# Kernel optimization log

Measured on AMD Instinct MI355X. Metric: run time of the kernel, lower is better.

The kernel has to match this reference:

```python
import jax, jax.numpy as jnp
import numpy as np

NEG_SLOPE = 0.2  # PyG GATv2Conv default
TOPK = 10        # hard-coded in original forward


def setup_inputs() -> dict:
    key = jax.random.key(0)
    N, E, D, L = 50000, 640000, 128, 3
    ks = jax.random.split(key, 12)
    s = 1.0 / np.sqrt(D)
    x = jax.random.normal(ks[0], (N, D), jnp.float32)
    edge_index = jax.random.randint(ks[1], (2, E), 0, N, dtype=jnp.int64)
    edge_attributes = jax.random.normal(ks[2], (E, D), jnp.float32)
    # GATv2 per-layer params (heads=1): lin_l (src), lin_r (dst), lin_edge, att, out bias
    Wl = jax.random.normal(ks[3], (L, D, D), jnp.float32) * s
    bl = jnp.zeros((L, D), jnp.float32)
    Wr = jax.random.normal(ks[4], (L, D, D), jnp.float32) * s
    br = jnp.zeros((L, D), jnp.float32)
    We = jax.random.normal(ks[5], (L, D, D), jnp.float32) * s
    att = jax.random.normal(ks[6], (L, D), jnp.float32) * s
    bias = jnp.zeros((L, D), jnp.float32)
    # final Conv1d(D, 1, 1) == linear projection D -> 1 per node
    Wf = jax.random.normal(ks[7], (D, 1), jnp.float32) * s
    bf = jnp.zeros((1,), jnp.float32)
    return {"x": x, "edge_index": edge_index, "edge_attributes": edge_attributes,
            "Wl": Wl, "bl": bl, "Wr": Wr, "br": br, "We": We, "att": att,
            "bias": bias, "Wf": Wf, "bf": bf}


def _gatv2_layer(x, src, dst, ea, N, Wl, bl, Wr, br, We, att, bias):
    xl = x @ Wl + bl            # [N, D] source transform
    xr = x @ Wr + br            # [N, D] target transform
    ee = ea @ We                # [E', D] edge transform (no bias in PyG lin_edge)
    m = jax.nn.leaky_relu(xl[src] + xr[dst] + ee, NEG_SLOPE)  # [E', D]
    logits = m @ att            # [E']
    # per-destination softmax (every node has a self-loop -> no empty segments)
    mx = jax.ops.segment_max(logits, dst, num_segments=N)
    w = jnp.exp(logits - mx[dst])
    den = jax.ops.segment_sum(w, dst, num_segments=N)
    alpha = w / den[dst]
    out = jax.ops.segment_sum(xl[src] * alpha[:, None], dst, num_segments=N)
    return out + bias


def reference(x, edge_index, edge_attributes, Wl, bl, Wr, br, We, att, bias, Wf, bf):
    N, D = x.shape
    src, dst = edge_index[0], edge_index[1]
    loop = jnp.arange(N, dtype=src.dtype)
    # add_self_loops with fill_value='mean': loop attr = mean of incoming edge attrs
    cnt = jax.ops.segment_sum(jnp.ones_like(dst, dtype=x.dtype), dst, num_segments=N)
    loop_attr = jax.ops.segment_sum(edge_attributes, dst, num_segments=N) / jnp.maximum(cnt, 1.0)[:, None]
    src_f = jnp.concatenate([src, loop])
    dst_f = jnp.concatenate([dst, loop])
    ea = jnp.concatenate([edge_attributes, loop_attr], axis=0)
    L = Wl.shape[0]
    for i in range(L):
        x = _gatv2_layer(x, src_f, dst_f, ea, N, Wl[i], bl[i], Wr[i], br[i], We[i], att[i], bias[i])
    scores = (x @ Wf)[:, 0] + bf[0]   # Conv1d(D,1,1): per-node scalar score [N]
    vals, idx = jax.lax.top_k(scores, TOPK)
    return vals, idx
```

## Files before the change

kernel.cpp:

```cpp
#include <hip/hip_runtime.h>
#include <hip/hip_bf16.h>
#include <float.h>

#define DD 128
#define NEG_SLOPE 0.2f
#define TKB 128

typedef __attribute__((ext_vector_type(8))) short bf16x8;
typedef __attribute__((ext_vector_type(4))) float f32x4;

__device__ __forceinline__ float lrelu(float v) {
    return fmaxf(v, 0.0f) + NEG_SLOPE * fminf(v, 0.0f);
}

__device__ __forceinline__ unsigned short f2bf(float f) {
    unsigned u = __float_as_uint(f);
    u += 0x7fff + ((u >> 16) & 1);
    return (unsigned short)(u >> 16);
}
__device__ __forceinline__ float bf2f(unsigned short h) {
    return __uint_as_float(((unsigned)h) << 16);
}


__global__ void k_hist(const int* __restrict__ dst, int E, int* __restrict__ cnt) {
    int i = blockIdx.x * blockDim.x + threadIdx.x;
    if (i < E) atomicAdd(&cnt[dst[i]], 1);
}

__global__ __launch_bounds__(1024) void k_scan(const int* __restrict__ cnt,
                                               int* __restrict__ row_ptr, int N) {
    __shared__ int sums[1024];
    int tid = threadIdx.x;
    int total = N + 1;
    int chunk = (total + 1023) / 1024;
    int lo = tid * chunk;
    int hi = min(lo + chunk, total);
    int s = 0;
    for (int i = lo; i < hi; ++i) s += (i < N) ? (cnt[i] + 1) : 0;
    sums[tid] = s;
    __syncthreads();
    for (int off = 1; off < 1024; off <<= 1) {
        int t = (tid >= off) ? sums[tid - off] : 0;
        __syncthreads();
        sums[tid] += t;
        __syncthreads();
    }
    int run = sums[tid] - s;
    for (int i = lo; i < hi; ++i) {
        row_ptr[i] = run;
        run += (i < N) ? (cnt[i] + 1) : 0;
    }
}

__global__ void k_scatter(const int* __restrict__ dst, int E, int N,
                          const int* __restrict__ row_ptr, int* __restrict__ fill,
                          const int* __restrict__ cnt, int* __restrict__ eids) {
    int i = blockIdx.x * blockDim.x + threadIdx.x;
    int tot = E + N;
    if (i >= tot) return;
    if (i < E) {
        int d = dst[i];
        int p = atomicAdd(&fill[d], 1);
        eids[row_ptr[d] + p] = i;
    } else {
        int n = i - E;
        eids[row_ptr[n] + cnt[n]] = E + n;
    }
}

__global__ void k_sort_rows(const int* __restrict__ row_ptr, int* __restrict__ eids, int N) {
    int n = blockIdx.x * blockDim.x + threadIdx.x;
    if (n >= N) return;
    int s = row_ptr[n], e = row_ptr[n + 1];
    for (int i = s + 1; i < e; ++i) {
        int v = eids[i];
        int j = i - 1;
        while (j >= s && eids[j] > v) { eids[j + 1] = eids[j]; --j; }
        eids[j + 1] = v;
    }
}

__global__ void k_invert(const int* __restrict__ eids, const int* __restrict__ srcArr,
                         int* __restrict__ pos, int* __restrict__ csr_src, int Etot, int E) {
    int p = blockIdx.x * blockDim.x + threadIdx.x;
    if (p >= Etot) return;
    int eid = eids[p];
    pos[eid] = p;
    csr_src[p] = (eid < E) ? srcArr[eid] : (eid - E);
}

__global__ __launch_bounds__(256) void k_loop_attr(const float* __restrict__ ea,
                                                   const int* __restrict__ row_ptr,
                                                   const int* __restrict__ cnt,
                                                   const int* __restrict__ eids,
                                                   float* __restrict__ loop_attr, int N) {
    int wid = (blockIdx.x * blockDim.x + threadIdx.x) >> 6;
    int lane = threadIdx.x & 63;
    if (wid >= N) return;
    int s = row_ptr[wid];
    int c = cnt[wid];
    float2 acc = make_float2(0.f, 0.f);
    for (int c0 = 0; c0 < c; c0 += 64) {
        int m = min(64, c - c0);
        int eid = 0;
        if (lane < m) eid = eids[s + c0 + lane];
        int p = 0;
        for (; p + 4 <= m; p += 4) {
            int e0 = __shfl(eid, p), e1 = __shfl(eid, p + 1);
            int e2 = __shfl(eid, p + 2), e3 = __shfl(eid, p + 3);
            float2 v0 = *reinterpret_cast<const float2*>(ea + (size_t)e0 * DD + 2 * lane);
            float2 v1 = *reinterpret_cast<const float2*>(ea + (size_t)e1 * DD + 2 * lane);
            float2 v2 = *reinterpret_cast<const float2*>(ea + (size_t)e2 * DD + 2 * lane);
            float2 v3 = *reinterpret_cast<const float2*>(ea + (size_t)e3 * DD + 2 * lane);
            acc.x += v0.x; acc.y += v0.y;
            acc.x += v1.x; acc.y += v1.y;
            acc.x += v2.x; acc.y += v2.y;
            acc.x += v3.x; acc.y += v3.y;
        }
        for (; p < m; ++p) {
            int e = __shfl(eid, p);
            float2 v = *reinterpret_cast<const float2*>(ea + (size_t)e * DD + 2 * lane);
            acc.x += v.x; acc.y += v.y;
        }
    }
    float inv = 1.0f / fmaxf((float)c, 1.0f);
    float2 o = make_float2(acc.x * inv, acc.y * inv);
    *reinterpret_cast<float2*>(loop_attr + (size_t)wid * DD + 2 * lane) = o;
}

__global__ void k_prepack(const float* __restrict__ W, unsigned short* __restrict__ WA, int L) {
    int idx = blockIdx.x * blockDim.x + threadIdx.x;
    int total = L * DD * DD;
    if (idx >= total) return;
    int l = idx >> 14;
    int rem = idx & 16383;
    int k = rem >> 7;
    int j = rem & 127;
    float w = W[(size_t)l * 16384 + (size_t)k * DD + j];
    unsigned short h = f2bf(w);
    unsigned short lo = f2bf(w - bf2f(h));
    int ks = k >> 5, g = (k >> 3) & 3, i = k & 7;
    size_t off = ((size_t)(ks * 4 + g) * DD + j) * 8 + i;
    unsigned short* base = WA + (size_t)l * 32768;
    base[off] = h;
    base[16384 + off] = lo;
}


__global__ __launch_bounds__(512, 2) void k_gemm_mfma(
    const float* __restrict__ X, const unsigned short* __restrict__ WA,
    const float* __restrict__ b, float* __restrict__ Y, int N) {

    __shared__ unsigned short WAs[32768];
    {
        const uint4* gsrc = reinterpret_cast<const uint4*>(WA);
        uint4* ldst = reinterpret_cast<uint4*>(WAs);
        int t = threadIdx.x;
        #pragma unroll
        for (int i = 0; i < 8; ++i) ldst[t + i * 512] = gsrc[t + i * 512];
    }
    __syncthreads();

    int tid  = threadIdx.x;
    int lane = tid & 63;
    int wv   = tid >> 6;
    int lc   = lane & 15;
    int g    = lane >> 4;

    int r0 = blockIdx.x * 256 + wv * 32;
    int rv[2]; bool ok[2];
    const float* rp[2];
    #pragma unroll
    for (int nf = 0; nf < 2; ++nf) {
        rv[nf] = r0 + nf * 16 + lc;
        ok[nf] = (rv[nf] < N);
        rp[nf] = X + (size_t)(ok[nf] ? rv[nf] : 0) * DD;
    }

    f32x4 acc[8][2];
    #pragma unroll
    for (int m = 0; m < 8; ++m)
        #pragma unroll
        for (int n = 0; n < 2; ++n)
            acc[m][n] = (f32x4){0.f, 0.f, 0.f, 0.f};

    float4 pr0[2], pr1[2];
    #pragma unroll
    for (int nf = 0; nf < 2; ++nf) {
        pr0[nf] = *reinterpret_cast<const float4*>(rp[nf] + g * 8);
        pr1[nf] = *reinterpret_cast<const float4*>(rp[nf] + g * 8 + 4);
    }

    #pragma unroll
    for (int ks = 0; ks < 4; ++ks) {
        bf16x8 Bh[2], Bl[2];
        #pragma unroll
        for (int nf = 0; nf < 2; ++nf) {
            float v[8] = {pr0[nf].x, pr0[nf].y, pr0[nf].z, pr0[nf].w,
                          pr1[nf].x, pr1[nf].y, pr1[nf].z, pr1[nf].w};
            #pragma unroll
            for (int i = 0; i < 8; ++i) {
                unsigned short h = f2bf(v[i]);
                Bh[nf][i] = (short)h;
                Bl[nf][i] = (short)f2bf(v[i] - bf2f(h));
            }
        }
        if (ks < 3) {
            int k0n = (ks + 1) * 32 + g * 8;
            #pragma unroll
            for (int nf = 0; nf < 2; ++nf) {
                pr0[nf] = *reinterpret_cast<const float4*>(rp[nf] + k0n);
                pr1[nf] = *reinterpret_cast<const float4*>(rp[nf] + k0n + 4);
            }
        }
        #pragma unroll
        for (int mf = 0; mf < 8; ++mf) {
            int aoff = ((ks * 4 + g) * DD + (mf * 16 + lc)) * 8;
            bf16x8 Ah = *reinterpret_cast<const bf16x8*>(&WAs[aoff]);
            bf16x8 Al = *reinterpret_cast<const bf16x8*>(&WAs[16384 + aoff]);
            #pragma unroll
            for (int nf = 0; nf < 2; ++nf) {
                acc[mf][nf] = __builtin_amdgcn_mfma_f32_16x16x32_bf16(Ah, Bh[nf], acc[mf][nf], 0, 0, 0);
                acc[mf][nf] = __builtin_amdgcn_mfma_f32_16x16x32_bf16(Al, Bh[nf], acc[mf][nf], 0, 0, 0);
                acc[mf][nf] = __builtin_amdgcn_mfma_f32_16x16x32_bf16(Ah, Bl[nf], acc[mf][nf], 0, 0, 0);
            }
        }
    }

    #pragma unroll
    for (int mf = 0; mf < 8; ++mf) {
        int f0 = mf * 16 + g * 4;
        float4 bv = *reinterpret_cast<const float4*>(b + f0);
        #pragma unroll
        for (int nf = 0; nf < 2; ++nf) {
            if (!ok[nf]) continue;
            float4 o;
            o.x = acc[mf][nf][0] + bv.x;
            o.y = acc[mf][nf][1] + bv.y;
            o.z = acc[mf][nf][2] + bv.z;
            o.w = acc[mf][nf][3] + bv.w;
            *reinterpret_cast<float4*>(Y + (size_t)rv[nf] * DD + f0) = o;
        }
    }
}

__global__ __launch_bounds__(512, 2) void k_edge_mfma(
    const float* __restrict__ ea, const float* __restrict__ loop_attr,
    const int* __restrict__ srcArr, const int* __restrict__ dstArr,
    const unsigned short* __restrict__ WA, const float* __restrict__ att,
    const float* __restrict__ xl, const float* __restrict__ xr,
    const int* __restrict__ pos, float* __restrict__ wlog, int E, int Etot) {

    __shared__ unsigned short WAs[32768];
    {
        const uint4* gsrc = reinterpret_cast<const uint4*>(WA);
        uint4* ldst = reinterpret_cast<uint4*>(WAs);
        int t = threadIdx.x;
        #pragma unroll
        for (int i = 0; i < 8; ++i) ldst[t + i * 512] = gsrc[t + i * 512];
    }
    __syncthreads();

    int tid  = threadIdx.x;
    int lane = tid & 63;
    int wv   = tid >> 6;
    int lc   = lane & 15;
    int g    = lane >> 4;

    int e0 = blockIdx.x * 256 + wv * 32;

    const float* rp[2];
    int ev[2]; bool ok[2];
    #pragma unroll
    for (int nf = 0; nf < 2; ++nf) {
        int e = e0 + nf * 16 + lc;
        ev[nf] = e;
        ok[nf] = (e < Etot);
        if (e < E)         rp[nf] = ea + (size_t)e * DD;
        else if (e < Etot) rp[nf] = loop_attr + (size_t)(e - E) * DD;
        else               rp[nf] = ea;
    }

    f32x4 acc[8][2];
    #pragma unroll
    for (int m = 0; m < 8; ++m)
        #pragma unroll
        for (int n = 0; n < 2; ++n)
            acc[m][n] = (f32x4){0.f, 0.f, 0.f, 0.f};

    float4 pr0[2], pr1[2];
    #pragma unroll
    for (int nf = 0; nf < 2; ++nf) {
        pr0[nf] = *reinterpret_cast<const float4*>(rp[nf] + g * 8);
        pr1[nf] = *reinterpret_cast<const float4*>(rp[nf] + g * 8 + 4);
    }

    #pragma unroll
    for (int ks = 0; ks < 4; ++ks) {
        bf16x8 Bh[2], Bl[2];
        #pragma unroll
        for (int nf = 0; nf < 2; ++nf) {
            float v[8] = {pr0[nf].x, pr0[nf].y, pr0[nf].z, pr0[nf].w,
                          pr1[nf].x, pr1[nf].y, pr1[nf].z, pr1[nf].w};
            #pragma unroll
            for (int i = 0; i < 8; ++i) {
                unsigned short h = f2bf(v[i]);
                Bh[nf][i] = (short)h;
                Bl[nf][i] = (short)f2bf(v[i] - bf2f(h));
            }
        }
        if (ks < 3) {
            int k0n = (ks + 1) * 32 + g * 8;
            #pragma unroll
            for (int nf = 0; nf < 2; ++nf) {
                pr0[nf] = *reinterpret_cast<const float4*>(rp[nf] + k0n);
                pr1[nf] = *reinterpret_cast<const float4*>(rp[nf] + k0n + 4);
            }
        }
        #pragma unroll
        for (int mf = 0; mf < 8; ++mf) {
            int aoff = ((ks * 4 + g) * DD + (mf * 16 + lc)) * 8;
            bf16x8 Ah = *reinterpret_cast<const bf16x8*>(&WAs[aoff]);
            bf16x8 Al = *reinterpret_cast<const bf16x8*>(&WAs[16384 + aoff]);
            #pragma unroll
            for (int nf = 0; nf < 2; ++nf) {
                acc[mf][nf] = __builtin_amdgcn_mfma_f32_16x16x32_bf16(Ah, Bh[nf], acc[mf][nf], 0, 0, 0);
                acc[mf][nf] = __builtin_amdgcn_mfma_f32_16x16x32_bf16(Al, Bh[nf], acc[mf][nf], 0, 0, 0);
                acc[mf][nf] = __builtin_amdgcn_mfma_f32_16x16x32_bf16(Ah, Bl[nf], acc[mf][nf], 0, 0, 0);
            }
        }
    }

    int sn[2], dn[2];
    #pragma unroll
    for (int nf = 0; nf < 2; ++nf) {
        int e = ev[nf];
        if (e < E)       { sn[nf] = srcArr[e]; dn[nf] = dstArr[e]; }
        else if (ok[nf]) { sn[nf] = e - E; dn[nf] = e - E; }
        else             { sn[nf] = 0; dn[nf] = 0; }
    }
    float partial[2] = {0.f, 0.f};
    #pragma unroll
    for (int mf = 0; mf < 8; ++mf) {
        int f0 = mf * 16 + g * 4;
        float4 attv = *reinterpret_cast<const float4*>(att + f0);
        #pragma unroll
        for (int nf = 0; nf < 2; ++nf) {
            float4 xlv = *reinterpret_cast<const float4*>(xl + (size_t)sn[nf] * DD + f0);
            float4 xrv = *reinterpret_cast<const float4*>(xr + (size_t)dn[nf] * DD + f0);
            float t0 = acc[mf][nf][0] + xlv.x + xrv.x;
            float t1 = acc[mf][nf][1] + xlv.y + xrv.y;
            float t2 = acc[mf][nf][2] + xlv.z + xrv.z;
            float t3 = acc[mf][nf][3] + xlv.w + xrv.w;
            partial[nf] += attv.x * lrelu(t0) + attv.y * lrelu(t1)
                         + attv.z * lrelu(t2) + attv.w * lrelu(t3);
        }
    }
    #pragma unroll
    for (int nf = 0; nf < 2; ++nf) {
        float p = partial[nf];
        p += __shfl_xor(p, 16);
        p += __shfl_xor(p, 32);
        if (lane < 16 && ok[nf]) wlog[pos[ev[nf]]] = p;
    }
}

__global__ __launch_bounds__(256) void k_sfx_agg(
    const float* __restrict__ wlog, const int* __restrict__ row_ptr,
    const int* __restrict__ csr_src, const float* __restrict__ xl,
    const float* __restrict__ bias, float* __restrict__ xout, int N) {
    int wid = (blockIdx.x * blockDim.x + threadIdx.x) >> 6;
    int lane = threadIdx.x & 63;
    if (wid >= N) return;
    int s = row_ptr[wid], e = row_ptr[wid + 1];
    float mx = -FLT_MAX;
    for (int c0 = s; c0 < e; c0 += 64) {
        float l = (c0 + lane < e) ? wlog[c0 + lane] : -FLT_MAX;
        l = fmaxf(l, __shfl_xor(l, 32));
        l = fmaxf(l, __shfl_xor(l, 16));
        l = fmaxf(l, __shfl_xor(l, 8));
        l = fmaxf(l, __shfl_xor(l, 4));
        l = fmaxf(l, __shfl_xor(l, 2));
        l = fmaxf(l, __shfl_xor(l, 1));
        mx = fmaxf(mx, l);
    }
    float den = 0.f;
    for (int c0 = s; c0 < e; c0 += 64) {
        float w = (c0 + lane < e) ? __expf(wlog[c0 + lane] - mx) : 0.f;
        w += __shfl_xor(w, 32);
        w += __shfl_xor(w, 16);
        w += __shfl_xor(w, 8);
        w += __shfl_xor(w, 4);
        w += __shfl_xor(w, 2);
        w += __shfl_xor(w, 1);
        den += w;
    }
    float inv = 1.0f / den;
    float2 acc = make_float2(0.f, 0.f);
    for (int c0 = s; c0 < e; c0 += 64) {
        int m = min(64, e - c0);
        float av = 0.f; int sv = 0;
        if (lane < m) {
            av = __expf(wlog[c0 + lane] - mx) * inv;
            sv = csr_src[c0 + lane];
        }
        int p = 0;
        for (; p + 4 <= m; p += 4) {
            float a0 = __shfl(av, p),     a1 = __shfl(av, p + 1);
            float a2 = __shfl(av, p + 2), a3 = __shfl(av, p + 3);
            int   r0 = __shfl(sv, p),     r1 = __shfl(sv, p + 1);
            int   r2 = __shfl(sv, p + 2), r3 = __shfl(sv, p + 3);
            float2 v0 = *reinterpret_cast<const float2*>(xl + (size_t)r0 * DD + 2 * lane);
            float2 v1 = *reinterpret_cast<const float2*>(xl + (size_t)r1 * DD + 2 * lane);
            float2 v2 = *reinterpret_cast<const float2*>(xl + (size_t)r2 * DD + 2 * lane);
            float2 v3 = *reinterpret_cast<const float2*>(xl + (size_t)r3 * DD + 2 * lane);
            acc.x += a0 * v0.x; acc.y += a0 * v0.y;
            acc.x += a1 * v1.x; acc.y += a1 * v1.y;
            acc.x += a2 * v2.x; acc.y += a2 * v2.y;
            acc.x += a3 * v3.x; acc.y += a3 * v3.y;
        }
        for (; p < m; ++p) {
            float ap = __shfl(av, p);
            int   rw = __shfl(sv, p);
            float2 v = *reinterpret_cast<const float2*>(xl + (size_t)rw * DD + 2 * lane);
            acc.x += ap * v.x;
            acc.y += ap * v.y;
        }
    }
    float2 bv = *reinterpret_cast<const float2*>(bias + 2 * lane);
    float2 o = make_float2(acc.x + bv.x, acc.y + bv.y);
    *reinterpret_cast<float2*>(xout + (size_t)wid * DD + 2 * lane) = o;
}


__global__ __launch_bounds__(256) void k_scores(const float* __restrict__ X,
                                                const float* __restrict__ Wf,
                                                const float* __restrict__ bf,
                                                float* __restrict__ scores, int N) {
    int gid = blockIdx.x * blockDim.x + threadIdx.x;
    int node = gid >> 6;
    int lane = threadIdx.x & 63;
    if (node >= N) return;
    float2 xv = *reinterpret_cast<const float2*>(&X[(size_t)node * DD + lane * 2]);
    float2 wv = *reinterpret_cast<const float2*>(&Wf[lane * 2]);
    float p = xv.x * wv.x + xv.y * wv.y;
    p += __shfl_xor(p, 32);
    p += __shfl_xor(p, 16);
    p += __shfl_xor(p, 8);
    p += __shfl_xor(p, 4);
    p += __shfl_xor(p, 2);
    p += __shfl_xor(p, 1);
    if (lane == 0) scores[node] = p + bf[0];
}

__device__ __forceinline__ bool tk_better(float a, int ai, float b, int bi) {
    return (a > b) || (a == b && ai < bi);
}

__device__ __forceinline__ void tk_insert(float sv, int si, float* v, int* ix) {
    if (tk_better(sv, si, v[9], ix[9])) {
        v[9] = sv; ix[9] = si;
        #pragma unroll
        for (int j = 9; j > 0; --j) {
            if (tk_better(v[j], ix[j], v[j - 1], ix[j - 1])) {
                float tv = v[j]; v[j] = v[j - 1]; v[j - 1] = tv;
                int ti = ix[j]; ix[j] = ix[j - 1]; ix[j - 1] = ti;
            }
        }
    }
}

__global__ __launch_bounds__(256) void k_topk1(const float* __restrict__ scores, int N,
                                               float* __restrict__ cand_v, int* __restrict__ cand_i) {
    __shared__ float lv[256 * 10];
    __shared__ int li[256 * 10];
    int t = threadIdx.x;
    float v[10]; int ix[10];
    #pragma unroll
    for (int j = 0; j < 10; ++j) { v[j] = -FLT_MAX; ix[j] = 0x7fffffff; }
    for (int i = blockIdx.x * 256 + t; i < N; i += TKB * 256)
        tk_insert(scores[i], i, v, ix);
    #pragma unroll
    for (int j = 0; j < 10; ++j) { lv[t * 10 + j] = v[j]; li[t * 10 + j] = ix[j]; }
    __syncthreads();
    for (int sh = 128; sh >= 1; sh >>= 1) {
        if (t < sh) {
            float bv[10]; int bi[10];
            #pragma unroll
            for (int j = 0; j < 10; ++j) { bv[j] = lv[(t + sh) * 10 + j]; bi[j] = li[(t + sh) * 10 + j]; }
            float mv[10]; int mi[10];
            int i1 = 0, i2 = 0;
            #pragma unroll
            for (int k = 0; k < 10; ++k) {
                if (tk_better(v[i1], ix[i1], bv[i2], bi[i2])) { mv[k] = v[i1]; mi[k] = ix[i1]; ++i1; }
                else { mv[k] = bv[i2]; mi[k] = bi[i2]; ++i2; }
            }
            #pragma unroll
            for (int j = 0; j < 10; ++j) {
                v[j] = mv[j]; ix[j] = mi[j];
                lv[t * 10 + j] = v[j]; li[t * 10 + j] = ix[j];
            }
        }
        __syncthreads();
    }
    if (t == 0) {
        #pragma unroll
        for (int j = 0; j < 10; ++j) {
            cand_v[blockIdx.x * 10 + j] = v[j];
            cand_i[blockIdx.x * 10 + j] = ix[j];
        }
    }
}

__global__ __launch_bounds__(64) void k_topk2(const float* __restrict__ cand_v,
                                              const int* __restrict__ cand_i,
                                              float* __restrict__ out) {
    __shared__ float lv[64 * 10];
    __shared__ int li[64 * 10];
    int t = threadIdx.x;
    float v[10]; int ix[10];
    #pragma unroll
    for (int j = 0; j < 10; ++j) { v[j] = -FLT_MAX; ix[j] = 0x7fffffff; }
    for (int i = t; i < TKB * 10; i += 64)
        tk_insert(cand_v[i], cand_i[i], v, ix);
    #pragma unroll
    for (int j = 0; j < 10; ++j) { lv[t * 10 + j] = v[j]; li[t * 10 + j] = ix[j]; }
    __syncthreads();
    for (int sh = 32; sh >= 1; sh >>= 1) {
        if (t < sh) {
            float bv[10]; int bi[10];
            #pragma unroll
            for (int j = 0; j < 10; ++j) { bv[j] = lv[(t + sh) * 10 + j]; bi[j] = li[(t + sh) * 10 + j]; }
            float mv[10]; int mi[10];
            int i1 = 0, i2 = 0;
            #pragma unroll
            for (int k = 0; k < 10; ++k) {
                if (tk_better(v[i1], ix[i1], bv[i2], bi[i2])) { mv[k] = v[i1]; mi[k] = ix[i1]; ++i1; }
                else { mv[k] = bv[i2]; mi[k] = bi[i2]; ++i2; }
            }
            #pragma unroll
            for (int j = 0; j < 10; ++j) {
                v[j] = mv[j]; ix[j] = mi[j];
                lv[t * 10 + j] = v[j]; li[t * 10 + j] = ix[j];
            }
        }
        __syncthreads();
    }
    if (t == 0) {
        #pragma unroll
        for (int j = 0; j < 10; ++j) {
            out[j] = v[j];
            out[10 + j] = (float)ix[j];
        }
    }
}


static inline size_t alignup(size_t v) { return (v + 255) & ~(size_t)255; }

extern "C" void kernel_launch(void* const* d_in, const int* in_sizes, int n_in,
                              void* d_out, int out_size, void* d_ws, size_t ws_size,
                              hipStream_t stream) {
    const float* x    = (const float*)d_in[0];
    const int*   ei   = (const int*)d_in[1];
    const float* ea   = (const float*)d_in[2];
    const float* Wl   = (const float*)d_in[3];
    const float* bl   = (const float*)d_in[4];
    const float* Wr   = (const float*)d_in[5];
    const float* br   = (const float*)d_in[6];
    const float* We   = (const float*)d_in[7];
    const float* att  = (const float*)d_in[8];
    const float* bias = (const float*)d_in[9];
    const float* Wf   = (const float*)d_in[10];
    const float* bf   = (const float*)d_in[11];

    int N = in_sizes[0] / DD;
    int E = in_sizes[1] / 2;
    int L = in_sizes[3] / (DD * DD);
    int Etot = E + N;
    const int* src = ei;
    const int* dst = ei + E;

    size_t off = 0;
    char* wsb = (char*)d_ws;
    auto carve = [&](size_t bytes) -> void* { void* p = wsb + off; off += alignup(bytes); return p; };
    unsigned short* WAe = (unsigned short*)carve((size_t)L * 32768 * 2);
    unsigned short* WAl = (unsigned short*)carve((size_t)L * 32768 * 2);
    unsigned short* WAr = (unsigned short*)carve((size_t)L * 32768 * 2);
    int*   cnt       = (int*)carve((size_t)N * 4);
    int*   fill      = (int*)carve((size_t)N * 4);
    int*   row_ptr   = (int*)carve((size_t)(N + 1) * 4);
    int*   eids      = (int*)carve((size_t)Etot * 4);
    int*   pos       = (int*)carve((size_t)Etot * 4);
    int*   csr_src   = (int*)carve((size_t)Etot * 4);
    float* wlog      = (float*)carve((size_t)Etot * 4);
    float* loop_attr = (float*)carve((size_t)N * DD * 4);
    float* xl        = (float*)carve((size_t)N * DD * 4);
    float* xr        = (float*)carve((size_t)N * DD * 4);
    float* xa        = (float*)carve((size_t)N * DD * 4);
    float* xb        = (float*)carve((size_t)N * DD * 4);
    float* scoresBuf = (float*)carve((size_t)N * 4);
    float* cand_v    = (float*)carve((size_t)TKB * 10 * 4);
    int*   cand_i    = (int*)carve((size_t)TKB * 10 * 4);
    (void)ws_size; (void)n_in; (void)out_size;

    hipMemsetAsync(cnt, 0, (size_t)N * 4, stream);
    hipMemsetAsync(fill, 0, (size_t)N * 4, stream);

    int ppBlocks = (L * DD * DD + 255) / 256;
    k_prepack<<<ppBlocks, 256, 0, stream>>>(We, WAe, L);
    k_prepack<<<ppBlocks, 256, 0, stream>>>(Wl, WAl, L);
    k_prepack<<<ppBlocks, 256, 0, stream>>>(Wr, WAr, L);
    k_hist<<<(E + 255) / 256, 256, 0, stream>>>(dst, E, cnt);
    k_scan<<<1, 1024, 0, stream>>>(cnt, row_ptr, N);
    k_scatter<<<(Etot + 255) / 256, 256, 0, stream>>>(dst, E, N, row_ptr, fill, cnt, eids);
    k_sort_rows<<<(N + 255) / 256, 256, 0, stream>>>(row_ptr, eids, N);
    k_invert<<<(Etot + 255) / 256, 256, 0, stream>>>(eids, src, pos, csr_src, Etot, E);
    int waveBlocks = (N * 64 + 255) / 256;
    k_loop_attr<<<waveBlocks, 256, 0, stream>>>(ea, row_ptr, cnt, eids, loop_attr, N);

    const float* xin = x;
    float* xout = xa;
    int gemmBlocks = (N + 255) / 256;
    int edgeBlocks = (Etot + 255) / 256;
    for (int l = 0; l < L; ++l) {
        k_gemm_mfma<<<gemmBlocks, 512, 0, stream>>>(xin, WAl + (size_t)l * 32768, bl + (size_t)l * DD, xl, N);
        k_gemm_mfma<<<gemmBlocks, 512, 0, stream>>>(xin, WAr + (size_t)l * 32768, br + (size_t)l * DD, xr, N);
        k_edge_mfma<<<edgeBlocks, 512, 0, stream>>>(ea, loop_attr, src, dst,
                                                    WAe + (size_t)l * 32768, att + (size_t)l * DD,
                                                    xl, xr, pos, wlog, E, Etot);
        k_sfx_agg<<<waveBlocks, 256, 0, stream>>>(wlog, row_ptr, csr_src, xl,
                                                  bias + (size_t)l * DD, xout, N);
        xin = xout;
        xout = (xout == xa) ? xb : xa;
    }
    k_scores<<<(N + 3) / 4, 256, 0, stream>>>(xin, Wf, bf, scoresBuf, N);
    k_topk1<<<TKB, 256, 0, stream>>>(scoresBuf, N, cand_v, cand_i);
    k_topk2<<<1, 64, 0, stream>>>(cand_v, cand_i, (float*)d_out);
}
```

Baseline: 1.221 ms.

## Fuse source/target node GEMMs and double per-wave edge tile

Merges the two per-layer node GEMMs (Wl and Wr) into one kernel that stages both packed weight matrices in LDS and reads each input row once, removing one launch and one full pass over x per layer. The edge transform kernel now processes 64 edges per wave instead of 32, amortising the weight-tile LDS load and A-fragment reads over twice as many MFMA ops. Both changes raise register pressure substantially (more accumulators), and the GEMM now uses 128 KB of LDS per block with relaxed launch bounds, which lowers occupancy and may cause spills.

```diff
diff --git a/kernel.cpp b/kernel.cpp
--- a/kernel.cpp
+++ b/kernel.cpp
@@ -148,9 +148,129 @@
 }
 
 
-__global__ __launch_bounds__(512, 2) void k_gemm_mfma(
-    const float* __restrict__ X, const unsigned short* __restrict__ WA,
-    const float* __restrict__ b, float* __restrict__ Y, int N) {
+__global__ __launch_bounds__(512) void k_gemm2(
+    const float* __restrict__ X,
+    const unsigned short* __restrict__ WAl, const unsigned short* __restrict__ WAr,
+    const float* __restrict__ bl, const float* __restrict__ br,
+    float* __restrict__ Yl, float* __restrict__ Yr, int N) {
+
+    __shared__ unsigned short WAs[65536];
+    {
+        const uint4* g1 = reinterpret_cast<const uint4*>(WAl);
+        const uint4* g2 = reinterpret_cast<const uint4*>(WAr);
+        uint4* l1 = reinterpret_cast<uint4*>(WAs);
+        uint4* l2 = reinterpret_cast<uint4*>(WAs + 32768);
+        int t = threadIdx.x;
+        #pragma unroll
+        for (int i = 0; i < 8; ++i) {
+            l1[t + i * 512] = g1[t + i * 512];
+            l2[t + i * 512] = g2[t + i * 512];
+        }
+    }
+    __syncthreads();
+
+    int tid  = threadIdx.x;
+    int lane = tid & 63;
+    int wv   = tid >> 6;
+    int lc   = lane & 15;
+    int g    = lane >> 4;
+
+    int r0 = blockIdx.x * 256 + wv * 32;
+    int rv[2]; bool ok[2];
+    const float* rp[2];
+    #pragma unroll
+    for (int nf = 0; nf < 2; ++nf) {
+        rv[nf] = r0 + nf * 16 + lc;
+        ok[nf] = (rv[nf] < N);
+        rp[nf] = X + (size_t)(ok[nf] ? rv[nf] : 0) * DD;
+    }
+
+    f32x4 accl[8][2], accr[8][2];
+    #pragma unroll
+    for (int m = 0; m < 8; ++m)
+        #pragma unroll
+        for (int n = 0; n < 2; ++n) {
+            accl[m][n] = (f32x4){0.f, 0.f, 0.f, 0.f};
+            accr[m][n] = (f32x4){0.f, 0.f, 0.f, 0.f};
+        }
+
+    float4 pr0[2], pr1[2];
+    #pragma unroll
+    for (int nf = 0; nf < 2; ++nf) {
+        pr0[nf] = *reinterpret_cast<const float4*>(rp[nf] + g * 8);
+        pr1[nf] = *reinterpret_cast<const float4*>(rp[nf] + g * 8 + 4);
+    }
+
+    #pragma unroll
+    for (int ks = 0; ks < 4; ++ks) {
+        bf16x8 Bh[2], Bl[2];
+        #pragma unroll
+        for (int nf = 0; nf < 2; ++nf) {
+            float v[8] = {pr0[nf].x, pr0[nf].y, pr0[nf].z, pr0[nf].w,
+                          pr1[nf].x, pr1[nf].y, pr1[nf].z, pr1[nf].w};
+            #pragma unroll
+            for (int i = 0; i < 8; ++i) {
+                unsigned short h = f2bf(v[i]);
+                Bh[nf][i] = (short)h;
+                Bl[nf][i] = (short)f2bf(v[i] - bf2f(h));
+            }
+        }
+        if (ks < 3) {
+            int k0n = (ks + 1) * 32 + g * 8;
+            #pragma unroll
+            for (int nf = 0; nf < 2; ++nf) {
+                pr0[nf] = *reinterpret_cast<const float4*>(rp[nf] + k0n);
+                pr1[nf] = *reinterpret_cast<const float4*>(rp[nf] + k0n + 4);
+            }
+        }
+        #pragma unroll
+        for (int mf = 0; mf < 8; ++mf) {
+            int aoff = ((ks * 4 + g) * DD + (mf * 16 + lc)) * 8;
+            bf16x8 Ahl = *reinterpret_cast<const bf16x8*>(&WAs[aoff]);
+            bf16x8 All = *reinterpret_cast<const bf16x8*>(&WAs[16384 + aoff]);
+            bf16x8 Ahr = *reinterpret_cast<const bf16x8*>(&WAs[32768 + aoff]);
+            bf16x8 Alr = *reinterpret_cast<const bf16x8*>(&WAs[49152 + aoff]);
+            #pragma unroll
+            for (int nf = 0; nf < 2; ++nf) {
+                accl[mf][nf] = __builtin_amdgcn_mfma_f32_16x16x32_bf16(Ahl, Bh[nf], accl[mf][nf], 0, 0, 0);
+                accl[mf][nf] = __builtin_amdgcn_mfma_f32_16x16x32_bf16(All, Bh[nf], accl[mf][nf], 0, 0, 0);
+                accl[mf][nf] = __builtin_amdgcn_mfma_f32_16x16x32_bf16(Ahl, Bl[nf], accl[mf][nf], 0, 0, 0);
+                accr[mf][nf] = __builtin_amdgcn_mfma_f32_16x16x32_bf16(Ahr, Bh[nf], accr[mf][nf], 0, 0, 0);
+                accr[mf][nf] = __builtin_amdgcn_mfma_f32_16x16x32_bf16(Alr, Bh[nf], accr[mf][nf], 0, 0, 0);
+                accr[mf][nf] = __builtin_amdgcn_mfma_f32_16x16x32_bf16(Ahr, Bl[nf], accr[mf][nf], 0, 0, 0);
+            }
+        }
+    }
+
+    #pragma unroll
+    for (int mf = 0; mf < 8; ++mf) {
+        int f0 = mf * 16 + g * 4;
+        float4 blv = *reinterpret_cast<const float4*>(bl + f0);
+        float4 brv = *reinterpret_cast<const float4*>(br + f0);
+        #pragma unroll
+        for (int nf = 0; nf < 2; ++nf) {
+            if (!ok[nf]) continue;
+            float4 o;
+            o.x = accl[mf][nf][0] + blv.x;
+            o.y = accl[mf][nf][1] + blv.y;
+            o.z = accl[mf][nf][2] + blv.z;
+            o.w = accl[mf][nf][3] + blv.w;
+            *reinterpret_cast<float4*>(Yl + (size_t)rv[nf] * DD + f0) = o;
+            o.x = accr[mf][nf][0] + brv.x;
+            o.y = accr[mf][nf][1] + brv.y;
+            o.z = accr[mf][nf][2] + brv.z;
+            o.w = accr[mf][nf][3] + brv.w;
+            *reinterpret_cast<float4*>(Yr + (size_t)rv[nf] * DD + f0) = o;
+        }
+    }
+}
+
+__global__ __launch_bounds__(512) void k_edge_mfma(
+    const float* __restrict__ ea, const float* __restrict__ loop_attr,
+    const int* __restrict__ srcArr, const int* __restrict__ dstArr,
+    const unsigned short* __restrict__ WA, const float* __restrict__ att,
+    const float* __restrict__ xl, const float* __restrict__ xr,
+    const int* __restrict__ pos, float* __restrict__ wlog, int E, int Etot) {
 
     __shared__ unsigned short WAs[32768];
     {
@@ -168,112 +288,12 @@
     int lc   = lane & 15;
     int g    = lane >> 4;
 
-    int r0 = blockIdx.x * 256 + wv * 32;
-    int rv[2]; bool ok[2];
-    const float* rp[2];
-    #pragma unroll
-    for (int nf = 0; nf < 2; ++nf) {
-        rv[nf] = r0 + nf * 16 + lc;
-        ok[nf] = (rv[nf] < N);
-        rp[nf] = X + (size_t)(ok[nf] ? rv[nf] : 0) * DD;
-    }
-
-    f32x4 acc[8][2];
-    #pragma unroll
-    for (int m = 0; m < 8; ++m)
-        #pragma unroll
-        for (int n = 0; n < 2; ++n)
-            acc[m][n] = (f32x4){0.f, 0.f, 0.f, 0.f};
-
-    float4 pr0[2], pr1[2];
-    #pragma unroll
-    for (int nf = 0; nf < 2; ++nf) {
-        pr0[nf] = *reinterpret_cast<const float4*>(rp[nf] + g * 8);
-        pr1[nf] = *reinterpret_cast<const float4*>(rp[nf] + g * 8 + 4);
-    }
-
-    #pragma unroll
-    for (int ks = 0; ks < 4; ++ks) {
-        bf16x8 Bh[2], Bl[2];
-        #pragma unroll
-        for (int nf = 0; nf < 2; ++nf) {
-            float v[8] = {pr0[nf].x, pr0[nf].y, pr0[nf].z, pr0[nf].w,
-                          pr1[nf].x, pr1[nf].y, pr1[nf].z, pr1[nf].w};
-            #pragma unroll
-            for (int i = 0; i < 8; ++i) {
-                unsigned short h = f2bf(v[i]);
-                Bh[nf][i] = (short)h;
-                Bl[nf][i] = (short)f2bf(v[i] - bf2f(h));
-            }
-        }
-        if (ks < 3) {
-            int k0n = (ks + 1) * 32 + g * 8;
-            #pragma unroll
-            for (int nf = 0; nf < 2; ++nf) {
-                pr0[nf] = *reinterpret_cast<const float4*>(rp[nf] + k0n);
-                pr1[nf] = *reinterpret_cast<const float4*>(rp[nf] + k0n + 4);
-            }
-        }
-        #pragma unroll
-        for (int mf = 0; mf < 8; ++mf) {
-            int aoff = ((ks * 4 + g) * DD + (mf * 16 + lc)) * 8;
-            bf16x8 Ah = *reinterpret_cast<const bf16x8*>(&WAs[aoff]);
-            bf16x8 Al = *reinterpret_cast<const bf16x8*>(&WAs[16384 + aoff]);
-            #pragma unroll
-            for (int nf = 0; nf < 2; ++nf) {
-                acc[mf][nf] = __builtin_amdgcn_mfma_f32_16x16x32_bf16(Ah, Bh[nf], acc[mf][nf], 0, 0, 0);
-                acc[mf][nf] = __builtin_amdgcn_mfma_f32_16x16x32_bf16(Al, Bh[nf], acc[mf][nf], 0, 0, 0);
-                acc[mf][nf] = __builtin_amdgcn_mfma_f32_16x16x32_bf16(Ah, Bl[nf], acc[mf][nf], 0, 0, 0);
-            }
-        }
-    }
-
-    #pragma unroll
-    for (int mf = 0; mf < 8; ++mf) {
-        int f0 = mf * 16 + g * 4;
-        float4 bv = *reinterpret_cast<const float4*>(b + f0);
-        #pragma unroll
-        for (int nf = 0; nf < 2; ++nf) {
-            if (!ok[nf]) continue;
-            float4 o;
-            o.x = acc[mf][nf][0] + bv.x;
-            o.y = acc[mf][nf][1] + bv.y;
-            o.z = acc[mf][nf][2] + bv.z;
-            o.w = acc[mf][nf][3] + bv.w;
-            *reinterpret_cast<float4*>(Y + (size_t)rv[nf] * DD + f0) = o;
-        }
-    }
-}
-
-__global__ __launch_bounds__(512, 2) void k_edge_mfma(
-    const float* __restrict__ ea, const float* __restrict__ loop_attr,
-    const int* __restrict__ srcArr, const int* __restrict__ dstArr,
-    const unsigned short* __restrict__ WA, const float* __restrict__ att,
-    const float* __restrict__ xl, const float* __restrict__ xr,
-    const int* __restrict__ pos, float* __restrict__ wlog, int E, int Etot) {
-
-    __shared__ unsigned short WAs[32768];
-    {
-        const uint4* gsrc = reinterpret_cast<const uint4*>(WA);
-        uint4* ldst = reinterpret_cast<uint4*>(WAs);
-        int t = threadIdx.x;
-        #pragma unroll
-        for (int i = 0; i < 8; ++i) ldst[t + i * 512] = gsrc[t + i * 512];
-    }
-    __syncthreads();
-
-    int tid  = threadIdx.x;
-    int lane = tid & 63;
-    int wv   = tid >> 6;
-    int lc   = lane & 15;
-    int g    = lane >> 4;
-
-    int e0 = blockIdx.x * 256 + wv * 32;
-
-    const float* rp[2];
-    int ev[2]; bool ok[2];
-    #pragma unroll
-    for (int nf = 0; nf < 2; ++nf) {
+    int e0 = blockIdx.x * 512 + wv * 64;
+
+    const float* rp[4];
+    int ev[4]; bool ok[4];
+    #pragma unroll
+    for (int nf = 0; nf < 4; ++nf) {
         int e = e0 + nf * 16 + lc;
         ev[nf] = e;
         ok[nf] = (e < Etot);
@@ -282,25 +302,25 @@
         else               rp[nf] = ea;
     }
 
-    f32x4 acc[8][2];
+    f32x4 acc[8][4];
     #pragma unroll
     for (int m = 0; m < 8; ++m)
         #pragma unroll
-        for (int n = 0; n < 2; ++n)
+        for (int n = 0; n < 4; ++n)
             acc[m][n] = (f32x4){0.f, 0.f, 0.f, 0.f};
 
-    float4 pr0[2], pr1[2];
-    #pragma unroll
-    for (int nf = 0; nf < 2; ++nf) {
+    float4 pr0[4], pr1[4];
+    #pragma unroll
+    for (int nf = 0; nf < 4; ++nf) {
         pr0[nf] = *reinterpret_cast<const float4*>(rp[nf] + g * 8);
         pr1[nf] = *reinterpret_cast<const float4*>(rp[nf] + g * 8 + 4);
     }
 
     #pragma unroll
     for (int ks = 0; ks < 4; ++ks) {
-        bf16x8 Bh[2], Bl[2];
-        #pragma unroll
-        for (int nf = 0; nf < 2; ++nf) {
+        bf16x8 Bh[4], Bl[4];
+        #pragma unroll
+        for (int nf = 0; nf < 4; ++nf) {
             float v[8] = {pr0[nf].x, pr0[nf].y, pr0[nf].z, pr0[nf].w,
                           pr1[nf].x, pr1[nf].y, pr1[nf].z, pr1[nf].w};
             #pragma unroll
@@ -313,7 +333,7 @@
         if (ks < 3) {
             int k0n = (ks + 1) * 32 + g * 8;
             #pragma unroll
-            for (int nf = 0; nf < 2; ++nf) {
+            for (int nf = 0; nf < 4; ++nf) {
                 pr0[nf] = *reinterpret_cast<const float4*>(rp[nf] + k0n);
                 pr1[nf] = *reinterpret_cast<const float4*>(rp[nf] + k0n + 4);
             }
@@ -324,7 +344,7 @@
             bf16x8 Ah = *reinterpret_cast<const bf16x8*>(&WAs[aoff]);
             bf16x8 Al = *reinterpret_cast<const bf16x8*>(&WAs[16384 + aoff]);
             #pragma unroll
-            for (int nf = 0; nf < 2; ++nf) {
+            for (int nf = 0; nf < 4; ++nf) {
                 acc[mf][nf] = __builtin_amdgcn_mfma_f32_16x16x32_bf16(Ah, Bh[nf], acc[mf][nf], 0, 0, 0);
                 acc[mf][nf] = __builtin_amdgcn_mfma_f32_16x16x32_bf16(Al, Bh[nf], acc[mf][nf], 0, 0, 0);
                 acc[mf][nf] = __builtin_amdgcn_mfma_f32_16x16x32_bf16(Ah, Bl[nf], acc[mf][nf], 0, 0, 0);
@@ -332,21 +352,21 @@
         }
     }
 
-    int sn[2], dn[2];
-    #pragma unroll
-    for (int nf = 0; nf < 2; ++nf) {
+    int sn[4], dn[4];
+    #pragma unroll
+    for (int nf = 0; nf < 4; ++nf) {
         int e = ev[nf];
         if (e < E)       { sn[nf] = srcArr[e]; dn[nf] = dstArr[e]; }
         else if (ok[nf]) { sn[nf] = e - E; dn[nf] = e - E; }
         else             { sn[nf] = 0; dn[nf] = 0; }
     }
-    float partial[2] = {0.f, 0.f};
+    float partial[4] = {0.f, 0.f, 0.f, 0.f};
     #pragma unroll
     for (int mf = 0; mf < 8; ++mf) {
         int f0 = mf * 16 + g * 4;
         float4 attv = *reinterpret_cast<const float4*>(att + f0);
         #pragma unroll
-        for (int nf = 0; nf < 2; ++nf) {
+        for (int nf = 0; nf < 4; ++nf) {
             float4 xlv = *reinterpret_cast<const float4*>(xl + (size_t)sn[nf] * DD + f0);
             float4 xrv = *reinterpret_cast<const float4*>(xr + (size_t)dn[nf] * DD + f0);
             float t0 = acc[mf][nf][0] + xlv.x + xrv.x;
@@ -358,7 +378,7 @@
         }
     }
     #pragma unroll
-    for (int nf = 0; nf < 2; ++nf) {
+    for (int nf = 0; nf < 4; ++nf) {
         float p = partial[nf];
         p += __shfl_xor(p, 16);
         p += __shfl_xor(p, 32);
@@ -623,10 +643,10 @@
     const float* xin = x;
     float* xout = xa;
     int gemmBlocks = (N + 255) / 256;
-    int edgeBlocks = (Etot + 255) / 256;
+    int edgeBlocks = (Etot + 511) / 512;
     for (int l = 0; l < L; ++l) {
-        k_gemm_mfma<<<gemmBlocks, 512, 0, stream>>>(xin, WAl + (size_t)l * 32768, bl + (size_t)l * DD, xl, N);
-        k_gemm_mfma<<<gemmBlocks, 512, 0, stream>>>(xin, WAr + (size_t)l * 32768, br + (size_t)l * DD, xr, N);
+        k_gemm2<<<gemmBlocks, 512, 0, stream>>>(xin, WAl + (size_t)l * 32768, WAr + (size_t)l * 32768,
+                                                bl + (size_t)l * DD, br + (size_t)l * DD, xl, xr, N);
         k_edge_mfma<<<edgeBlocks, 512, 0, stream>>>(ea, loop_attr, src, dst,
                                                     WAe + (size_t)l * 32768, att + (size_t)l * DD,
                                                     xl, xr, pos, wlog, E, Etot);
```

Result: slower. 1.594 ms (+30.5%).
